# Kernel optimization log

Hardware: AMD Instinct MI355X
Metric: run time of the kernel (lower is better)

## Reference

```python
import jax, jax.numpy as jnp
import numpy as np

B, T, V = 4, 2048, 2048
D, H, L = 512, 8, 4
HD = D // H


def setup_inputs() -> dict:
    key = jax.random.key(0)
    ks = jax.random.split(key, 8)
    inp = {
        "x": jax.random.normal(ks[0], (B, T, V), dtype=jnp.float32),
        "token_embedding": jax.random.normal(ks[1], (D, V), dtype=jnp.float32),
        "position_embedding": jax.random.normal(ks[2], (T, D), dtype=jnp.float32),
        "Wk": jax.random.normal(ks[3], (L, D, D), dtype=jnp.float32),
        "Wq": jax.random.normal(ks[4], (L, D, D), dtype=jnp.float32),
        "Wv": jax.random.normal(ks[5], (L, D, D), dtype=jnp.float32),
        "Wp": jax.random.normal(ks[6], (L, D, D), dtype=jnp.float32),
        "readout": jax.random.normal(ks[7], (V, D), dtype=jnp.float32),
    }
    return inp


def _attention_block(h, wk, wq, wv, wp):
    # h: [B, T, D]; weights [D, D] (inner_dim == D since head_dim*num_heads == D)
    b, t, c = h.shape
    s = c ** (-0.5)

    def proj(w):
        # F.linear(h, w) = h @ w.T -> [B,T,D] -> [B,H,T,HD], scaled by C^{-1/2}
        return (jnp.einsum('btc,dc->btd', h, w) * s).reshape(b, t, H, HD).transpose(0, 2, 1, 3)

    q, k, v = proj(wq), proj(wk), proj(wv)
    scores = jnp.einsum('bhqd,bhkd->bhqk', q, k) * (HD ** (-0.5))  # [B,H,T,T]
    attn = jax.nn.softmax(scores, axis=-1)
    out = jnp.einsum('bhqk,bhkd->bhqd', attn, v)  # [B,H,T,HD]
    out = out.transpose(0, 2, 1, 3).reshape(b, t, c)
    # projection.size(-1) == inner_dim == D
    return jnp.einsum('btc,oc->bto', out, wp) * (c ** (-0.5))


def reference(x, token_embedding, position_embedding, Wk, Wq, Wv, Wp, readout):
    b, t, c = x.shape  # c == vocab_size
    tok = jnp.einsum('btv,dv->btd', x, token_embedding) * (c ** (-0.5))
    h = tok + position_embedding[:t]
    for l in range(L):
        h = _attention_block(h, Wk[l], Wq[l], Wv[l], Wp[l])
    # logits on last token; readout.size(-1) == D
    logits = jnp.einsum('bd,vd->bv', h[:, -1, :], readout) * (D ** (-0.5))
    return logits
```

## Files before the change

### kernel.cpp

```cpp
#include <hip/hip_runtime.h>
#include <math.h>

typedef __attribute__((ext_vector_type(4))) float    f32x4;
typedef __attribute__((ext_vector_type(2))) _Float16 f16x2;
typedef __attribute__((ext_vector_type(4))) _Float16 f16x4;
typedef __attribute__((ext_vector_type(8))) _Float16 f16x8;

constexpr int Bc  = 4;
constexpr int Tc  = 2048;
constexpr int Vc  = 2048;
constexpr int Dc  = 512;
constexpr int Hc  = 8;
constexpr int HDc = 64;
constexpr int Lc  = 4;
constexpr size_t SZe = (size_t)Bc * Tc * Dc;

constexpr float SM_C = 12.0f;

__device__ __forceinline__ void gload_lds16(const _Float16* g, _Float16* s) {
    __builtin_amdgcn_global_load_lds(
        (const __attribute__((address_space(1))) void*)g,
        (__attribute__((address_space(3))) void*)s,
        16, 0, 0);
}

__device__ __forceinline__ f16x2 cvt_pk(float a, float b) {
    return __builtin_bit_cast(f16x2, __builtin_amdgcn_cvt_pkrtz(a, b));
}

__global__ __launch_bounds__(256) void cvt_k(
    const float* __restrict__ in, _Float16* __restrict__ out, int n4)
{
    for (int i = blockIdx.x * 256 + threadIdx.x; i < n4; i += gridDim.x * 256) {
        float4 v = ((const float4*)in)[i];
        f16x4 h = {(_Float16)v.x, (_Float16)v.y, (_Float16)v.z, (_Float16)v.w};
        *(f16x4*)&out[(size_t)i * 4] = h;
    }
}

template<bool QKV>
__global__ __launch_bounds__(256) void gemm_f16(
    const _Float16* __restrict__ A,
    const _Float16* __restrict__ W0, const _Float16* __restrict__ W1,
    const _Float16* __restrict__ W2,
    void* __restrict__ C0, const float* __restrict__ pos,
    int K, float scA, float scB)
{
    __shared__ __align__(16) _Float16 LA[2][128 * 64];
    __shared__ __align__(16) _Float16 LB[2][64 * 64];

    const int tid = threadIdx.x;
    const int w  = tid >> 6, l = tid & 63;
    const int li = l & 15,  lg = l >> 4;
    const int wm = w >> 1,  wn = w & 1;
    const int m0 = blockIdx.x * 128;

    int sec = 0, n0;
    const _Float16* Wb;
    if (QKV) {
        sec = blockIdx.y >> 3; n0 = (blockIdx.y & 7) * 64;
        Wb = (sec == 0) ? W0 : ((sec == 1) ? W1 : W2);
    } else {
        n0 = blockIdx.y * 64; Wb = W0;
    }
    const float scale = (sec == 0) ? scA : scB;

    const _Float16* srcA[4];
    const _Float16* srcB[2];
#pragma unroll
    for (int i = 0; i < 4; ++i) {
        const int d = i * 4096 + tid * 16;
        const int r = d >> 7, cb = (d & 127) ^ ((r & 7) << 4);
        srcA[i] = A + (size_t)(m0 + r) * K + (cb >> 1);
    }
#pragma unroll
    for (int i = 0; i < 2; ++i) {
        const int d = i * 4096 + tid * 16;
        const int r = d >> 7, cb = (d & 127) ^ ((r & 7) << 4);
        srcB[i] = Wb + (size_t)(n0 + r) * K + (cb >> 1);
    }

    auto stage = [&](int b) {
#pragma unroll
        for (int i = 0; i < 4; ++i) { gload_lds16(srcA[i], &LA[b][i * 2048 + tid * 8]); srcA[i] += 64; }
#pragma unroll
        for (int i = 0; i < 2; ++i) { gload_lds16(srcB[i], &LB[b][i * 2048 + tid * 8]); srcB[i] += 64; }
    };

    f32x4 acc[4][2];
#pragma unroll
    for (int i = 0; i < 4; ++i)
#pragma unroll
        for (int j = 0; j < 2; ++j) acc[i][j] = (f32x4){0.f, 0.f, 0.f, 0.f};

    auto compute = [&](int b) {
        const char* Ab = (const char*)&LA[b][0];
        const char* Bb = (const char*)&LB[b][0];
        f16x8 af[4][2], bf[2][2];
#pragma unroll
        for (int mb = 0; mb < 4; ++mb) {
            const int row = wm * 64 + mb * 16 + li, sz = (row & 7) << 4;
#pragma unroll
            for (int fi = 0; fi < 2; ++fi)
                af[mb][fi] = *(const f16x8*)(Ab + row * 128 + ((fi * 64 + lg * 16) ^ sz));
        }
#pragma unroll
        for (int nb = 0; nb < 2; ++nb) {
            const int row = wn * 32 + nb * 16 + li, sz = (row & 7) << 4;
#pragma unroll
            for (int fi = 0; fi < 2; ++fi)
                bf[nb][fi] = *(const f16x8*)(Bb + row * 128 + ((fi * 64 + lg * 16) ^ sz));
        }
#pragma unroll
        for (int mb = 0; mb < 4; ++mb)
#pragma unroll
            for (int nb = 0; nb < 2; ++nb)
#pragma unroll
                for (int fi = 0; fi < 2; ++fi)
                    acc[mb][nb] = __builtin_amdgcn_mfma_f32_16x16x32_f16(
                        af[mb][fi], bf[nb][fi], acc[mb][nb], 0, 0, 0);
    };

    const int NTk = K >> 6;
    stage(0);
    for (int kt = 0; kt < NTk; ++kt) {
        const int cur = kt & 1;
        if (kt + 1 < NTk) {
            stage(cur ^ 1);
            asm volatile("s_waitcnt vmcnt(6)" ::: "memory");
        } else {
            asm volatile("s_waitcnt vmcnt(0)" ::: "memory");
        }
        __builtin_amdgcn_s_barrier();
        __builtin_amdgcn_sched_barrier(0);
        compute(cur);
        __builtin_amdgcn_s_barrier();
        __builtin_amdgcn_sched_barrier(0);
    }

#pragma unroll
    for (int mb = 0; mb < 4; ++mb) {
#pragma unroll
        for (int nb = 0; nb < 2; ++nb) {
            const int mbase = m0 + wm * 64 + mb * 16 + lg * 4;
            const int nc    = n0 + wn * 32 + nb * 16 + li;
            if (QKV && sec == 2) {
                const int bb2 = mbase >> 11, t0 = mbase & (Tc - 1);
                const int hh2 = nc >> 6,     dd = nc & 63;
                f16x4 vv;
#pragma unroll
                for (int r = 0; r < 4; ++r) vv[r] = (_Float16)(acc[mb][nb][r] * scale);
                _Float16* vt = (_Float16*)C0 + 2 * SZe;
                *(f16x4*)&vt[(((size_t)bb2 * Hc + hh2) * HDc + dd) * Tc + t0] = vv;
            } else if (QKV) {
                _Float16* outp = (_Float16*)C0 + (size_t)sec * SZe;
#pragma unroll
                for (int r = 0; r < 4; ++r) {
                    const int m = mbase + r, bb2 = m >> 11, t = m & (Tc - 1);
                    outp[(((size_t)bb2 * Hc + (nc >> 6)) * Tc + t) * HDc + (nc & 63)] =
                        (_Float16)(acc[mb][nb][r] * scale);
                }
            } else {
                _Float16* outp = (_Float16*)C0;
#pragma unroll
                for (int r = 0; r < 4; ++r) {
                    const int m = mbase + r;
                    float val = acc[mb][nb][r] * scale;
                    if (pos) val += pos[(size_t)(m & (Tc - 1)) * Dc + nc];
                    outp[(size_t)m * Dc + nc] = (_Float16)val;
                }
            }
        }
    }
}

__global__ __launch_bounds__(256) void attn_mfma(
    const _Float16* __restrict__ Qh, const _Float16* __restrict__ Kh,
    const _Float16* __restrict__ Vt, _Float16* __restrict__ o)
{
    __shared__ __align__(16) _Float16 Ks[2][64 * 64];
    __shared__ __align__(16) _Float16 Vs[2][64 * 64];

    const int bid = blockIdx.x;
    const int qt  = bid & 31;
    const int bh  = bid >> 5;
    const int hh  = bh & (Hc - 1);
    const int bb  = bh >> 3;
    const int w   = threadIdx.x >> 6;
    const int l   = threadIdx.x & 63;
    const int li  = l & 15, lg = l >> 4;
    const int q0  = qt * 64 + w * 16;
    const int swz = (li & 7) << 4;

    const _Float16* Qb = Qh + (size_t)bh * Tc * HDc;
    const _Float16* Kb = Kh + (size_t)bh * Tc * HDc;
    const _Float16* Vb = Vt + (size_t)bh * HDc * Tc;

    f16x8 qf[2];
#pragma unroll
    for (int fi = 0; fi < 2; ++fi)
        qf[fi] = *(const f16x8*)&Qb[(size_t)(q0 + li) * HDc + fi * 32 + lg * 8];

    const int off0 = w * 2048 + l * 16;
    const int off1 = off0 + 1024;
    const int r0 = off0 >> 7, cs0 = (off0 & 127) ^ ((r0 & 7) << 4);
    const int r1 = off1 >> 7, cs1 = (off1 & 127) ^ ((r1 & 7) << 4);
    const _Float16* sK0 = Kb + r0 * HDc + (cs0 >> 1);
    const _Float16* sK1 = Kb + r1 * HDc + (cs1 >> 1);
    const _Float16* sV0 = Vb + (size_t)r0 * Tc + (cs0 >> 1);
    const _Float16* sV1 = Vb + (size_t)r1 * Tc + (cs1 >> 1);

    auto stage = [&](int b) {
        gload_lds16(sK0, &Ks[b][w * 1024]);
        gload_lds16(sK1, &Ks[b][w * 1024 + 512]);
        gload_lds16(sV0, &Vs[b][w * 1024]);
        gload_lds16(sV1, &Vs[b][w * 1024 + 512]);
        sK0 += 64 * HDc; sK1 += 64 * HDc;
        sV0 += 64;       sV1 += 64;
    };

    f32x4 oacc[4];
#pragma unroll
    for (int dt = 0; dt < 4; ++dt) oacc[dt] = (f32x4){0.f, 0.f, 0.f, 0.f};
    float lrun = 0.f;

    stage(0);
    constexpr int NT = Tc / 64;
    for (int kt = 0; kt < NT; ++kt) {
        const int cur = kt & 1;
        if (kt + 1 < NT) {
            stage(cur ^ 1);
            asm volatile("s_waitcnt vmcnt(4)" ::: "memory");
        } else {
            asm volatile("s_waitcnt vmcnt(0)" ::: "memory");
        }
        __builtin_amdgcn_s_barrier();
        __builtin_amdgcn_sched_barrier(0);

        const char* KL = (const char*)&Ks[cur][0];
        const char* VL = (const char*)&Vs[cur][0];

        f32x4 s[4];
        __builtin_amdgcn_s_setprio(1);
#pragma unroll
        for (int t = 0; t < 4; ++t) {
            s[t] = (f32x4){-SM_C, -SM_C, -SM_C, -SM_C};
            const char* kr = KL + (t * 16 + li) * 128;
#pragma unroll
            for (int fi = 0; fi < 2; ++fi) {
                f16x8 kf = *(const f16x8*)(kr + ((fi * 64 + lg * 16) ^ swz));
                s[t] = __builtin_amdgcn_mfma_f32_16x16x32_f16(kf, qf[fi], s[t], 0, 0, 0);
            }
        }
        __builtin_amdgcn_s_setprio(0);

        float p[16];
#pragma unroll
        for (int t = 0; t < 4; ++t)
#pragma unroll
            for (int r = 0; r < 4; ++r)
                p[t * 4 + r] = __builtin_amdgcn_exp2f(s[t][r]);

        float ps0 = (p[0] + p[1]) + (p[2] + p[3]);
        float ps1 = (p[4] + p[5]) + (p[6] + p[7]);
        float ps2 = (p[8] + p[9]) + (p[10] + p[11]);
        float ps3 = (p[12] + p[13]) + (p[14] + p[15]);
        lrun += (ps0 + ps1) + (ps2 + ps3);

        f16x4 pf[4];
#pragma unroll
        for (int t = 0; t < 4; ++t) {
            f16x2 lo = cvt_pk(p[t * 4 + 0], p[t * 4 + 1]);
            f16x2 hi = cvt_pk(p[t * 4 + 2], p[t * 4 + 3]);
            pf[t] = (f16x4){lo[0], lo[1], hi[0], hi[1]};
        }

        __builtin_amdgcn_s_setprio(1);
#pragma unroll
        for (int dt = 0; dt < 4; ++dt) {
            const char* vr = VL + (dt * 16 + li) * 128;
#pragma unroll
            for (int t = 0; t < 4; ++t) {
                f16x4 vf = *(const f16x4*)(vr + ((t * 32 + lg * 8) ^ swz));
                oacc[dt] = __builtin_amdgcn_mfma_f32_16x16x16f16(vf, pf[t], oacc[dt], 0, 0, 0);
            }
        }
        __builtin_amdgcn_s_setprio(0);

        __builtin_amdgcn_s_barrier();
        __builtin_amdgcn_sched_barrier(0);
    }

    lrun += __shfl_xor(lrun, 16);
    lrun += __shfl_xor(lrun, 32);

    const float inv = 1.f / lrun;
    _Float16* op = o + ((size_t)(bb * Tc + q0 + li) * Dc + hh * HDc + lg * 4);
#pragma unroll
    for (int dt = 0; dt < 4; ++dt) {
        f16x4 rv = {(_Float16)(oacc[dt][0] * inv), (_Float16)(oacc[dt][1] * inv),
                    (_Float16)(oacc[dt][2] * inv), (_Float16)(oacc[dt][3] * inv)};
        *(f16x4*)(op + dt * 16) = rv;
    }
}

__global__ __launch_bounds__(256) void readout_k(
    const _Float16* __restrict__ h, const float* __restrict__ ro,
    float* __restrict__ out, float scale)
{
    const int idx = blockIdx.x * 256 + threadIdx.x;
    const int vv  = idx & (Vc - 1);
    const int bb  = idx >> 11;
    const _Float16* hp = h + (size_t)(bb * Tc + (Tc - 1)) * Dc;
    const float* rp = ro + (size_t)vv * Dc;
    float ax = 0.f, ay = 0.f, az = 0.f, aw = 0.f;
#pragma unroll 8
    for (int i = 0; i < Dc / 4; ++i) {
        f16x4  hv = *(const f16x4*)(hp + i * 4);
        float4 rv = *(const float4*)(rp + i * 4);
        ax = fmaf((float)hv[0], rv.x, ax);
        ay = fmaf((float)hv[1], rv.y, ay);
        az = fmaf((float)hv[2], rv.z, az);
        aw = fmaf((float)hv[3], rv.w, aw);
    }
    out[idx] = ((ax + ay) + (az + aw)) * scale;
}

extern "C" void kernel_launch(void* const* d_in, const int* in_sizes, int n_in,
                              void* d_out, int out_size, void* d_ws, size_t ws_size,
                              hipStream_t stream)
{
    const float* x    = (const float*)d_in[0];
    const float* temb = (const float*)d_in[1];
    const float* pemb = (const float*)d_in[2];
    const float* Wk   = (const float*)d_in[3];
    const float* Wq   = (const float*)d_in[4];
    const float* Wv   = (const float*)d_in[5];
    const float* Wp   = (const float*)d_in[6];
    const float* ro   = (const float*)d_in[7];
    float* out = (float*)d_out;

    _Float16* h16    = (_Float16*)d_ws;
    _Float16* temb16 = h16 + SZe;
    _Float16* wq16   = temb16 + (size_t)Dc * Vc;
    _Float16* wk16   = wq16 + (size_t)Lc * Dc * Dc;
    _Float16* wv16   = wk16 + (size_t)Lc * Dc * Dc;
    _Float16* wp16   = wv16 + (size_t)Lc * Dc * Dc;
    _Float16* o16    = wp16 + (size_t)Lc * Dc * Dc;
    _Float16* qh     = o16 + SZe;
    _Float16* kh     = qh + SZe;
    _Float16* vt     = kh + SZe;
    _Float16* x16    = o16;

    const float s_emb  = 1.0f / sqrtf((float)Vc);
    const float s_proj = 1.0f / sqrtf((float)Dc);
    const float s_q    = s_proj * 0.125f * 1.44269504f;

    const int W4 = Lc * Dc * Dc / 4;
    cvt_k<<<2048, 256, 0, stream>>>(x, x16, (int)(SZe));
    cvt_k<<<1024, 256, 0, stream>>>(temb, temb16, Dc * Vc / 4);
    cvt_k<<<1024, 256, 0, stream>>>(Wq, wq16, W4);
    cvt_k<<<1024, 256, 0, stream>>>(Wk, wk16, W4);
    cvt_k<<<1024, 256, 0, stream>>>(Wv, wv16, W4);
    cvt_k<<<1024, 256, 0, stream>>>(Wp, wp16, W4);

    gemm_f16<false><<<dim3(64, 8), 256, 0, stream>>>(
        x16, temb16, nullptr, nullptr, h16, pemb, Vc, s_emb, s_emb);

    const size_t WOFF = (size_t)Dc * Dc;
    for (int lyr = 0; lyr < Lc; ++lyr) {
        gemm_f16<true><<<dim3(64, 24), 256, 0, stream>>>(
            h16, wq16 + lyr * WOFF, wk16 + lyr * WOFF, wv16 + lyr * WOFF,
            qh, nullptr, Dc, s_q, s_proj);

        attn_mfma<<<Bc * Hc * (Tc / 64), 256, 0, stream>>>(qh, kh, vt, o16);

        gemm_f16<false><<<dim3(64, 8), 256, 0, stream>>>(
            o16, wp16 + lyr * WOFF, nullptr, nullptr, h16, nullptr, Dc, s_proj, s_proj);
    }

    readout_k<<<(Bc * Vc) / 256, 256, 0, stream>>>(h16, ro, out, s_proj);
}
```

Measured before the change: 432.3 us.

## Widen GEMM tiles, MFMA row-sum in attention, reorder blocks, merge weight conversions

The GEMM block tile grows from 128x64 to 128x128, so each wave computes 64x64 and reuses its A fragments across twice as many MFMAs. This halves the grid and doubles LDS use for B. In attention, the softmax row sum is now accumulated with an MFMA against a vector of ones on the f16 probabilities, replacing scalar adds and cross-lane shuffles. Attention blocks are reordered so that consecutive blocks walk across heads rather than query tiles, and the four weight conversions become one launch. Smaller grids (256 blocks for the projection GEMM) may underfill the GPU, and summing f16-rounded probabilities slightly changes numerics.

```diff
diff --git a/kernel.cpp b/kernel.cpp
--- a/kernel.cpp
+++ b/kernel.cpp
@@ -38,6 +38,26 @@
     }
 }
 
+__global__ __launch_bounds__(256) void cvtW_k(
+    const float* __restrict__ a, const float* __restrict__ b,
+    const float* __restrict__ c, const float* __restrict__ d,
+    _Float16* __restrict__ oa, _Float16* __restrict__ ob,
+    _Float16* __restrict__ oc, _Float16* __restrict__ od, int n4)
+{
+    const float* in; _Float16* out;
+    switch (blockIdx.y) {
+        case 0:  in = a; out = oa; break;
+        case 1:  in = b; out = ob; break;
+        case 2:  in = c; out = oc; break;
+        default: in = d; out = od; break;
+    }
+    for (int i = blockIdx.x * 256 + threadIdx.x; i < n4; i += gridDim.x * 256) {
+        float4 v = ((const float4*)in)[i];
+        f16x4 h = {(_Float16)v.x, (_Float16)v.y, (_Float16)v.z, (_Float16)v.w};
+        *(f16x4*)&out[(size_t)i * 4] = h;
+    }
+}
+
 template<bool QKV>
 __global__ __launch_bounds__(256) void gemm_f16(
     const _Float16* __restrict__ A,
@@ -47,7 +67,7 @@
     int K, float scA, float scB)
 {
     __shared__ __align__(16) _Float16 LA[2][128 * 64];
-    __shared__ __align__(16) _Float16 LB[2][64 * 64];
+    __shared__ __align__(16) _Float16 LB[2][128 * 64];
 
     const int tid = threadIdx.x;
     const int w  = tid >> 6, l = tid & 63;
@@ -58,25 +78,20 @@
     int sec = 0, n0;
     const _Float16* Wb;
     if (QKV) {
-        sec = blockIdx.y >> 3; n0 = (blockIdx.y & 7) * 64;
+        sec = blockIdx.y >> 2; n0 = (blockIdx.y & 3) * 128;
         Wb = (sec == 0) ? W0 : ((sec == 1) ? W1 : W2);
     } else {
-        n0 = blockIdx.y * 64; Wb = W0;
+        n0 = blockIdx.y * 128; Wb = W0;
     }
     const float scale = (sec == 0) ? scA : scB;
 
     const _Float16* srcA[4];
-    const _Float16* srcB[2];
+    const _Float16* srcB[4];
 #pragma unroll
     for (int i = 0; i < 4; ++i) {
         const int d = i * 4096 + tid * 16;
         const int r = d >> 7, cb = (d & 127) ^ ((r & 7) << 4);
-        srcA[i] = A + (size_t)(m0 + r) * K + (cb >> 1);
-    }
-#pragma unroll
-    for (int i = 0; i < 2; ++i) {
-        const int d = i * 4096 + tid * 16;
-        const int r = d >> 7, cb = (d & 127) ^ ((r & 7) << 4);
+        srcA[i] = A  + (size_t)(m0 + r) * K + (cb >> 1);
         srcB[i] = Wb + (size_t)(n0 + r) * K + (cb >> 1);
     }
 
@@ -84,19 +99,19 @@
 #pragma unroll
         for (int i = 0; i < 4; ++i) { gload_lds16(srcA[i], &LA[b][i * 2048 + tid * 8]); srcA[i] += 64; }
 #pragma unroll
-        for (int i = 0; i < 2; ++i) { gload_lds16(srcB[i], &LB[b][i * 2048 + tid * 8]); srcB[i] += 64; }
+        for (int i = 0; i < 4; ++i) { gload_lds16(srcB[i], &LB[b][i * 2048 + tid * 8]); srcB[i] += 64; }
     };
 
-    f32x4 acc[4][2];
+    f32x4 acc[4][4];
 #pragma unroll
     for (int i = 0; i < 4; ++i)
 #pragma unroll
-        for (int j = 0; j < 2; ++j) acc[i][j] = (f32x4){0.f, 0.f, 0.f, 0.f};
+        for (int j = 0; j < 4; ++j) acc[i][j] = (f32x4){0.f, 0.f, 0.f, 0.f};
 
     auto compute = [&](int b) {
         const char* Ab = (const char*)&LA[b][0];
         const char* Bb = (const char*)&LB[b][0];
-        f16x8 af[4][2], bf[2][2];
+        f16x8 af[4][2], bf[4][2];
 #pragma unroll
         for (int mb = 0; mb < 4; ++mb) {
             const int row = wm * 64 + mb * 16 + li, sz = (row & 7) << 4;
@@ -105,8 +120,8 @@
                 af[mb][fi] = *(const f16x8*)(Ab + row * 128 + ((fi * 64 + lg * 16) ^ sz));
         }
 #pragma unroll
-        for (int nb = 0; nb < 2; ++nb) {
-            const int row = wn * 32 + nb * 16 + li, sz = (row & 7) << 4;
+        for (int nb = 0; nb < 4; ++nb) {
+            const int row = wn * 64 + nb * 16 + li, sz = (row & 7) << 4;
 #pragma unroll
             for (int fi = 0; fi < 2; ++fi)
                 bf[nb][fi] = *(const f16x8*)(Bb + row * 128 + ((fi * 64 + lg * 16) ^ sz));
@@ -114,7 +129,7 @@
 #pragma unroll
         for (int mb = 0; mb < 4; ++mb)
 #pragma unroll
-            for (int nb = 0; nb < 2; ++nb)
+            for (int nb = 0; nb < 4; ++nb)
 #pragma unroll
                 for (int fi = 0; fi < 2; ++fi)
                     acc[mb][nb] = __builtin_amdgcn_mfma_f32_16x16x32_f16(
@@ -127,7 +142,7 @@
         const int cur = kt & 1;
         if (kt + 1 < NTk) {
             stage(cur ^ 1);
-            asm volatile("s_waitcnt vmcnt(6)" ::: "memory");
+            asm volatile("s_waitcnt vmcnt(8)" ::: "memory");
         } else {
             asm volatile("s_waitcnt vmcnt(0)" ::: "memory");
         }
@@ -141,9 +156,9 @@
 #pragma unroll
     for (int mb = 0; mb < 4; ++mb) {
 #pragma unroll
-        for (int nb = 0; nb < 2; ++nb) {
+        for (int nb = 0; nb < 4; ++nb) {
             const int mbase = m0 + wm * 64 + mb * 16 + lg * 4;
-            const int nc    = n0 + wn * 32 + nb * 16 + li;
+            const int nc    = n0 + wn * 64 + nb * 16 + li;
             if (QKV && sec == 2) {
                 const int bb2 = mbase >> 11, t0 = mbase & (Tc - 1);
                 const int hh2 = nc >> 6,     dd = nc & 63;
@@ -182,8 +197,8 @@
     __shared__ __align__(16) _Float16 Vs[2][64 * 64];
 
     const int bid = blockIdx.x;
-    const int qt  = bid & 31;
-    const int bh  = bid >> 5;
+    const int bh  = bid & 31;
+    const int qt  = bid >> 5;
     const int hh  = bh & (Hc - 1);
     const int bb  = bh >> 3;
     const int w   = threadIdx.x >> 6;
@@ -222,7 +237,8 @@
     f32x4 oacc[4];
 #pragma unroll
     for (int dt = 0; dt < 4; ++dt) oacc[dt] = (f32x4){0.f, 0.f, 0.f, 0.f};
-    float lrun = 0.f;
+    f32x4 lacc = (f32x4){0.f, 0.f, 0.f, 0.f};
+    const f16x4 ones = (f16x4){(_Float16)1.f, (_Float16)1.f, (_Float16)1.f, (_Float16)1.f};
 
     stage(0);
     constexpr int NT = Tc / 64;
@@ -254,28 +270,22 @@
         }
         __builtin_amdgcn_s_setprio(0);
 
-        float p[16];
+        f16x4 pf[4];
+#pragma unroll
+        for (int t = 0; t < 4; ++t) {
+            float p0 = __builtin_amdgcn_exp2f(s[t][0]);
+            float p1 = __builtin_amdgcn_exp2f(s[t][1]);
+            float p2 = __builtin_amdgcn_exp2f(s[t][2]);
+            float p3 = __builtin_amdgcn_exp2f(s[t][3]);
+            f16x2 lo = cvt_pk(p0, p1);
+            f16x2 hi = cvt_pk(p2, p3);
+            pf[t] = (f16x4){lo[0], lo[1], hi[0], hi[1]};
+        }
+
+        __builtin_amdgcn_s_setprio(1);
 #pragma unroll
         for (int t = 0; t < 4; ++t)
-#pragma unroll
-            for (int r = 0; r < 4; ++r)
-                p[t * 4 + r] = __builtin_amdgcn_exp2f(s[t][r]);
-
-        float ps0 = (p[0] + p[1]) + (p[2] + p[3]);
-        float ps1 = (p[4] + p[5]) + (p[6] + p[7]);
-        float ps2 = (p[8] + p[9]) + (p[10] + p[11]);
-        float ps3 = (p[12] + p[13]) + (p[14] + p[15]);
-        lrun += (ps0 + ps1) + (ps2 + ps3);
-
-        f16x4 pf[4];
-#pragma unroll
-        for (int t = 0; t < 4; ++t) {
-            f16x2 lo = cvt_pk(p[t * 4 + 0], p[t * 4 + 1]);
-            f16x2 hi = cvt_pk(p[t * 4 + 2], p[t * 4 + 3]);
-            pf[t] = (f16x4){lo[0], lo[1], hi[0], hi[1]};
-        }
-
-        __builtin_amdgcn_s_setprio(1);
+            lacc = __builtin_amdgcn_mfma_f32_16x16x16f16(ones, pf[t], lacc, 0, 0, 0);
 #pragma unroll
         for (int dt = 0; dt < 4; ++dt) {
             const char* vr = VL + (dt * 16 + li) * 128;
@@ -291,10 +301,7 @@
         __builtin_amdgcn_sched_barrier(0);
     }
 
-    lrun += __shfl_xor(lrun, 16);
-    lrun += __shfl_xor(lrun, 32);
-
-    const float inv = 1.f / lrun;
+    const float inv = 1.f / lacc[0];
     _Float16* op = o + ((size_t)(bb * Tc + q0 + li) * Dc + hh * HDc + lg * 4);
 #pragma unroll
     for (int dt = 0; dt < 4; ++dt) {
@@ -357,25 +364,23 @@
     const float s_q    = s_proj * 0.125f * 1.44269504f;
 
     const int W4 = Lc * Dc * Dc / 4;
-    cvt_k<<<2048, 256, 0, stream>>>(x, x16, (int)(SZe));
-    cvt_k<<<1024, 256, 0, stream>>>(temb, temb16, Dc * Vc / 4);
-    cvt_k<<<1024, 256, 0, stream>>>(Wq, wq16, W4);
-    cvt_k<<<1024, 256, 0, stream>>>(Wk, wk16, W4);
-    cvt_k<<<1024, 256, 0, stream>>>(Wv, wv16, W4);
-    cvt_k<<<1024, 256, 0, stream>>>(Wp, wp16, W4);
-
-    gemm_f16<false><<<dim3(64, 8), 256, 0, stream>>>(
+    cvt_k<<<2048, 256, 0, stream>>>(x, x16, (int)SZe);
+    cvt_k<<<512, 256, 0, stream>>>(temb, temb16, Dc * Vc / 4);
+    cvtW_k<<<dim3(512, 4), 256, 0, stream>>>(Wq, Wk, Wv, Wp,
+                                             wq16, wk16, wv16, wp16, W4);
+
+    gemm_f16<false><<<dim3(64, 4), 256, 0, stream>>>(
         x16, temb16, nullptr, nullptr, h16, pemb, Vc, s_emb, s_emb);
 
     const size_t WOFF = (size_t)Dc * Dc;
     for (int lyr = 0; lyr < Lc; ++lyr) {
-        gemm_f16<true><<<dim3(64, 24), 256, 0, stream>>>(
+        gemm_f16<true><<<dim3(64, 12), 256, 0, stream>>>(
             h16, wq16 + lyr * WOFF, wk16 + lyr * WOFF, wv16 + lyr * WOFF,
             qh, nullptr, Dc, s_q, s_proj);
 
         attn_mfma<<<Bc * Hc * (Tc / 64), 256, 0, stream>>>(qh, kh, vt, o16);
 
-        gemm_f16<false><<<dim3(64, 8), 256, 0, stream>>>(
+        gemm_f16<false><<<dim3(64, 4), 256, 0, stream>>>(
             o16, wp16 + lyr * WOFF, nullptr, nullptr, h16, nullptr, Dc, s_proj, s_proj);
     }
 
```

Result: slower. 454.3 us (+5.1%).
